# Kernel tuning notes

Hardware: AMD Instinct MI355X
Metric: run time of the kernel (lower is better)

The kernel has to match this reference:

```python
import jax, jax.numpy as jnp
import numpy as np
import math

B, T_TOK, D, H, L, V, NC, BS = 8, 511, 768, 12, 8, 512, 10, 512

PARAM_NAMES = ['tok_emb','cond_emb','type_emb','pos_emb','ln1_g','ln1_b','Wq','bq','Wk','bk','Wv','bv','Wp','bp','ln2_g','ln2_b','W1','b1','W2','b2','lnf_g','lnf_b','head_w']


def setup_inputs() -> dict:
    key = jax.random.key(0)
    ks = iter(jax.random.split(key, 40))
    def w(shape):
        return jax.random.normal(next(ks), shape, jnp.float32) * 0.02
    inp = {
        'idx': jax.random.randint(next(ks), (B, T_TOK), 0, V),
        'condition': jax.random.randint(next(ks), (B,), 0, NC + 1),
        'tok_emb': w((V, D)),
        'cond_emb': w((NC + 1, D)),
        'type_emb': w((2, D)),
        'pos_emb': w((1, BS, D)),
        'ln1_g': jnp.ones((L, D)), 'ln1_b': jnp.zeros((L, D)),
        'Wq': w((L, D, D)), 'bq': jnp.zeros((L, D)),
        'Wk': w((L, D, D)), 'bk': jnp.zeros((L, D)),
        'Wv': w((L, D, D)), 'bv': jnp.zeros((L, D)),
        'Wp': w((L, D, D)), 'bp': jnp.zeros((L, D)),
        'ln2_g': jnp.ones((L, D)), 'ln2_b': jnp.zeros((L, D)),
        'W1': w((L, D, 4 * D)), 'b1': jnp.zeros((L, 4 * D)),
        'W2': w((L, 4 * D, D)), 'b2': jnp.zeros((L, D)),
        'lnf_g': jnp.ones((D,)), 'lnf_b': jnp.zeros((D,)),
        'head_w': w((D, V)),
    }
    return inp


def _ln(x, g, b):
    m = x.mean(-1, keepdims=True)
    v = ((x - m) ** 2).mean(-1, keepdims=True)
    return (x - m) * jax.lax.rsqrt(v + 1e-5) * g + b


def _forward(idx, condition, p):
    b, t = idx.shape
    T = t + 1  # conditioning token prepended
    x = jnp.concatenate([p['cond_emb'][condition][:, None, :], p['tok_emb'][idx]], axis=1)
    type_ids = jnp.concatenate([jnp.zeros((1,), jnp.int32), jnp.ones((t,), jnp.int32)])
    x = x + p['pos_emb'][:, :T] + p['type_emb'][type_ids][None]
    dh = D // H
    causal = jnp.tril(jnp.ones((T, T), bool))

    def block(x, lp):
        ln1_g, ln1_b, Wq, bq, Wk, bk, Wv, bv, Wp, bp, ln2_g, ln2_b, W1, b1, W2, b2 = lp
        h = _ln(x, ln1_g, ln1_b)
        def heads(W, bias):
            return (h @ W + bias).reshape(b, T, H, dh).transpose(0, 2, 1, 3)  # [b,H,T,dh]
        q, k, v = heads(Wq, bq), heads(Wk, bk), heads(Wv, bv)
        att = jnp.einsum('bhqd,bhkd->bhqk', q, k) * (1.0 / math.sqrt(dh))
        att = jax.nn.softmax(jnp.where(causal, att, -jnp.inf), axis=-1)
        y = jnp.einsum('bhqk,bhkd->bhqd', att, v).transpose(0, 2, 1, 3).reshape(b, T, D)
        # NOTE: original Block applies ln1 in-place, so residual base is post-ln h
        x = h + (y @ Wp + bp)
        h2 = _ln(x, ln2_g, ln2_b)
        x = x + (jax.nn.gelu(h2 @ W1 + b1, approximate=False) @ W2 + b2)
        return x, None

    lp = (p['ln1_g'], p['ln1_b'], p['Wq'], p['bq'], p['Wk'], p['bk'], p['Wv'], p['bv'],
          p['Wp'], p['bp'], p['ln2_g'], p['ln2_b'], p['W1'], p['b1'], p['W2'], p['b2'])
    x, _ = jax.lax.scan(block, x, lp)
    logits = _ln(x, p['lnf_g'], p['lnf_b']) @ p['head_w']
    return logits[:, 1:, :]  # strip conditioning position (cond_len=1)


def reference(idx, condition, tok_emb, cond_emb, type_emb, pos_emb, ln1_g, ln1_b, Wq, bq, Wk, bk, Wv, bv, Wp, bp, ln2_g, ln2_b, W1, b1, W2, b2, lnf_g, lnf_b, head_w):
    p = dict(zip(PARAM_NAMES, (tok_emb, cond_emb, type_emb, pos_emb, ln1_g, ln1_b, Wq, bq, Wk, bk, Wv, bv, Wp, bp, ln2_g, ln2_b, W1, b1, W2, b2, lnf_g, lnf_b, head_w)))
    return _forward(idx, condition, p)
```

## Files before the change

kernel.cpp:

```cpp
#include <hip/hip_runtime.h>
#include <hip/hip_bf16.h>
#include <cstddef>
#include <cstdint>


#define NTOK 4096
#define TSEQ 512
#define DMODEL 768
#define DFF 3072
#define NHEAD 12
#define DHEAD 64
#define NLAYER 8
#define VOCAB 512
#define QKVD 2304

typedef __attribute__((ext_vector_type(8))) __bf16 bf16x8;
typedef __attribute__((ext_vector_type(4))) float f32x4;
typedef __attribute__((ext_vector_type(4))) unsigned int u32x4;
typedef __attribute__((ext_vector_type(4))) unsigned short u16x4;

__device__ __forceinline__ unsigned short f2bf(float f) {
  union { float f; unsigned int u; } v; v.f = f;
  return (unsigned short)((v.u + 0x7FFFu + ((v.u >> 16) & 1u)) >> 16);
}

__device__ __forceinline__ float gelu_exact(float x) {
  return 0.5f * x * (1.f + erff(x * 0.70710678118654752f));
}

__device__ __forceinline__ void gload_lds16(const void* g, void* lds) {
  __builtin_amdgcn_global_load_lds(
      reinterpret_cast<__attribute__((address_space(1))) void*>(
          reinterpret_cast<uintptr_t>(g)),
      reinterpret_cast<__attribute__((address_space(3))) void*>(
          reinterpret_cast<uintptr_t>(lds)),
      16, 0, 0);
}

template <int N>
__device__ __forceinline__ void waitvm() {
  if constexpr (N == 0) asm volatile("s_waitcnt vmcnt(0)" ::: "memory");
  else if constexpr (N == 2) asm volatile("s_waitcnt vmcnt(2)" ::: "memory");
  else if constexpr (N == 3) asm volatile("s_waitcnt vmcnt(3)" ::: "memory");
  else if constexpr (N == 4) asm volatile("s_waitcnt vmcnt(4)" ::: "memory");
  else static_assert(N == 0, "unsupported vmcnt");
}

__global__ __launch_bounds__(256) void embed_k(
    const int* __restrict__ idx, const int* __restrict__ cond,
    const float* __restrict__ tok, const float* __restrict__ ce,
    const float* __restrict__ te, const float* __restrict__ pe,
    float* __restrict__ X) {
  int row = blockIdx.x;
  int b = row >> 9, t = row & 511;
  int tid = threadIdx.x;
  const float* src = (t == 0) ? (ce + (size_t)cond[b] * DMODEL)
                              : (tok + (size_t)idx[b * 511 + t - 1] * DMODEL);
  const float* ty = te + (t != 0 ? DMODEL : 0);
  const float* pp = pe + (size_t)t * DMODEL;
  float* dst = X + (size_t)row * DMODEL;
#pragma unroll
  for (int i = 0; i < 3; i++) {
    int d = tid + i * 256;
    dst[d] = src[d] + pp[d] + ty[d];
  }
}

template <bool F32OUT>
__global__ __launch_bounds__(256) void ln_k(
    const float* __restrict__ X, const float* __restrict__ g,
    const float* __restrict__ bta, float* __restrict__ O,
    unsigned short* __restrict__ Ob) {
  const int row = blockIdx.x;
  const int tid = threadIdx.x;
  const float* x = X + (size_t)row * DMODEL;
  float v0 = x[tid], v1 = x[tid + 256], v2 = x[tid + 512];
  float s = v0 + v1 + v2;
  float ss = v0 * v0 + v1 * v1 + v2 * v2;
#pragma unroll
  for (int o = 32; o > 0; o >>= 1) {
    s += __shfl_down(s, o);
    ss += __shfl_down(ss, o);
  }
  __shared__ float sm[8];
  const int wid = tid >> 6, lane = tid & 63;
  if (lane == 0) { sm[wid] = s; sm[wid + 4] = ss; }
  __syncthreads();
  float st = sm[0] + sm[1] + sm[2] + sm[3];
  float sst = sm[4] + sm[5] + sm[6] + sm[7];
  float mean = st * (1.f / DMODEL);
  float var = sst * (1.f / DMODEL) - mean * mean;
  float rstd = rsqrtf(var + 1e-5f);
  float y0 = (v0 - mean) * rstd * g[tid] + bta[tid];
  float y1 = (v1 - mean) * rstd * g[tid + 256] + bta[tid + 256];
  float y2 = (v2 - mean) * rstd * g[tid + 512] + bta[tid + 512];
  if (F32OUT) {
    float* o = O + (size_t)row * DMODEL;
    o[tid] = y0; o[tid + 256] = y1; o[tid + 512] = y2;
  }
  unsigned short* ob = Ob + (size_t)row * DMODEL;
  ob[tid] = f2bf(y0); ob[tid + 256] = f2bf(y1); ob[tid + 512] = f2bf(y2);
}

struct P4 { const float* p[4]; };

__global__ __launch_bounds__(256) void transp_k(P4 src,
                                                unsigned short* __restrict__ out,
                                                int K, int N) {
  __shared__ alignas(16) float Ls[64][65];
  const float* W = src.p[blockIdx.z];
  unsigned short* o = out + (size_t)blockIdx.z * K * N;
  const int tid = threadIdx.x;
  const int n0 = blockIdx.x * 64, k0 = blockIdx.y * 64;
  const int r = tid >> 4, c4 = (tid & 15) * 4;
#pragma unroll
  for (int i = 0; i < 4; i++) {
    const int kk = r + i * 16;
    const float4 v = *(const float4*)(W + (size_t)(k0 + kk) * N + n0 + c4);
    Ls[c4 + 0][kk] = v.x;
    Ls[c4 + 1][kk] = v.y;
    Ls[c4 + 2][kk] = v.z;
    Ls[c4 + 3][kk] = v.w;
  }
  __syncthreads();
#pragma unroll
  for (int i = 0; i < 4; i++) {
    const int nn = r + i * 16;
    u16x4 q;
    q.x = f2bf(Ls[nn][c4 + 0]);
    q.y = f2bf(Ls[nn][c4 + 1]);
    q.z = f2bf(Ls[nn][c4 + 2]);
    q.w = f2bf(Ls[nn][c4 + 3]);
    *(u16x4*)(o + (size_t)(n0 + nn) * K + k0 + c4) = q;
  }
}

__global__ __launch_bounds__(256) void packb_k(const float* __restrict__ bq,
                                               const float* __restrict__ bk,
                                               const float* __restrict__ bv,
                                               float* __restrict__ o) {
  const int l = blockIdx.x, tid = threadIdx.x;
#pragma unroll
  for (int i = 0; i < 9; i++) {
    int n = tid + i * 256;
    float v = (n < 768) ? bq[l * 768 + n]
                        : (n < 1536) ? bk[l * 768 + n - 768]
                                     : bv[l * 768 + n - 1536];
    o[l * QKVD + n] = v;
  }
}

#define BK 32

constexpr int EPQ = 0;
constexpr int EPRES = 1;
constexpr int EPGELU = 2;
constexpr int EPHEAD = 3;
constexpr int EPQB = 4;

template <int EP, int TBM, int TBN>
__global__ __launch_bounds__(256) void mm_k(
    const unsigned short* __restrict__ A, const unsigned short* __restrict__ Bt,
    const float* __restrict__ bias, const float* __restrict__ res,
    void* __restrict__ Cv, int K, int N) {
  __shared__ alignas(16) unsigned short As[3][TBM * BK];
  __shared__ alignas(16) unsigned short Bs[3][TBN * BK];
  constexpr int WM = TBM / 2, WN = TBN / 2;
  constexpr int MI = WM / 16, NJ = WN / 16;
  constexpr int GA = TBM / 64, GB = TBN / 64;
  constexpr int G = GA + GB;
  const int tid = threadIdx.x;
  const int lane = tid & 63, wid = tid >> 6;
  const int wr = wid >> 1, wc = wid & 1;
  const int m0 = blockIdx.x * TBM, n0 = blockIdx.y * TBN;

  f32x4 acc[MI][NJ];
#pragma unroll
  for (int i = 0; i < MI; i++)
#pragma unroll
    for (int j = 0; j < NJ; j++) acc[i][j] = f32x4{0.f, 0.f, 0.f, 0.f};

  const int srow = lane >> 2;
  const int gch = (lane & 3) ^ ((srow >> 1) & 3);
  const size_t rb = (size_t)K * 2;
  const int fr = lane & 15, ks = lane >> 4;
  const int NKI = K / BK;

  auto stage = [&](int kt, int slot) {
    const size_t koff = (size_t)kt * BK * 2;
#pragma unroll
    for (int t = 0; t < GA; t++) {
      const int rr = wid * (TBM / 4) + t * 16;
      gload_lds16((const char*)A + (size_t)(m0 + rr + srow) * rb + koff + gch * 16,
                  &As[slot][rr * BK]);
    }
#pragma unroll
    for (int t = 0; t < GB; t++) {
      const int rr = wid * (TBN / 4) + t * 16;
      gload_lds16((const char*)Bt + (size_t)(n0 + rr + srow) * rb + koff + gch * 16,
                  &Bs[slot][rr * BK]);
    }
  };

  stage(0, 0);
  stage(1, 1);
  waitvm<G>();
  __builtin_amdgcn_s_barrier();
  __builtin_amdgcn_sched_barrier(0);

  int cur = 0;
  for (int t = 0; t < NKI; ++t) {
    const unsigned short* Ab = &As[cur][0];
    const unsigned short* Bb = &Bs[cur][0];
    u32x4 ar[MI], br[NJ];
#pragma unroll
    for (int i = 0; i < MI; i++) {
      const int ra = wr * WM + i * 16 + fr;
      ar[i] = *(const u32x4*)((const char*)Ab + ra * 64 +
                              ((ks ^ ((ra >> 1) & 3)) << 4));
    }
#pragma unroll
    for (int j = 0; j < NJ; j++) {
      const int rbw = wc * WN + j * 16 + fr;
      br[j] = *(const u32x4*)((const char*)Bb + rbw * 64 +
                              ((ks ^ ((rbw >> 1) & 3)) << 4));
    }
    const int nslot = (cur >= 1) ? cur - 1 : cur + 2;
    const bool pf = (t + 2 < NKI);
    if (pf) stage(t + 2, nslot);
    __builtin_amdgcn_s_setprio(1);
#pragma unroll
    for (int i = 0; i < MI; i++)
#pragma unroll
      for (int j = 0; j < NJ; j++)
        acc[i][j] = __builtin_amdgcn_mfma_f32_16x16x32_bf16(
            __builtin_bit_cast(bf16x8, ar[i]), __builtin_bit_cast(bf16x8, br[j]),
            acc[i][j], 0, 0, 0);
    __builtin_amdgcn_s_setprio(0);
    if (pf) waitvm<G>(); else waitvm<0>();
    __builtin_amdgcn_sched_barrier(0);
    __builtin_amdgcn_s_barrier();
    __builtin_amdgcn_sched_barrier(0);
    cur = (cur == 2) ? 0 : cur + 1;
  }

#pragma unroll
  for (int i = 0; i < MI; i++) {
#pragma unroll
    for (int j = 0; j < NJ; j++) {
      const int n = n0 + wc * WN + j * 16 + fr;
      float bv = 0.f;
      if (EP != EPHEAD) bv = bias[n];
#pragma unroll
      for (int r = 0; r < 4; r++) {
        const int m = m0 + wr * WM + i * 16 + ks * 4 + r;
        float v = acc[i][j][r] + bv;
        if (EP == EPRES) v += res[(size_t)m * N + n];
        if (EP == EPGELU) {
          ((unsigned short*)Cv)[(size_t)m * N + n] = f2bf(gelu_exact(v));
        } else if (EP == EPQB) {
          ((unsigned short*)Cv)[(size_t)m * N + n] = f2bf(v);
        } else if (EP == EPHEAD) {
          const int bb = m >> 9, tt = m & 511;
          if (tt)
            ((float*)Cv)[(size_t)(bb * 511 + tt - 1) * N + n] = v;
        } else {
          ((float*)Cv)[(size_t)m * N + n] = v;
        }
      }
    }
  }
}

__global__ __launch_bounds__(256) void attn_mfma_k(
    const unsigned short* __restrict__ QKV, unsigned short* __restrict__ Y) {
  __shared__ alignas(16) unsigned short Ks[64][72];
  __shared__ alignas(16) unsigned short Vt[64][72];
  __shared__ alignas(16) unsigned short Pl[4][16][72];
  const int qt = 7 - (int)blockIdx.x;
  const int h = blockIdx.y, b = blockIdx.z;
  const int tid = threadIdx.x;
  const int lane = tid & 63, wq = tid >> 6;
  const int fr = lane & 15, g = lane >> 4;

  const size_t qrow =
      (size_t)(b * TSEQ + qt * 64 + wq * 16 + fr) * QKVD + h * DHEAD;
  u32x4 qf[2];
  qf[0] = *(const u32x4*)(QKV + qrow + g * 8);
  qf[1] = *(const u32x4*)(QKV + qrow + 32 + g * 8);

  f32x4 of[4];
  float m[4], l[4];
#pragma unroll
  for (int jd = 0; jd < 4; jd++) of[jd] = f32x4{0.f, 0.f, 0.f, 0.f};
#pragma unroll
  for (int r = 0; r < 4; r++) { m[r] = -1e30f; l[r] = 0.f; }

  const int srow = tid >> 2, sc = (tid & 3) * 16;

  for (int kt = 0; kt <= qt; kt++) {
    {
      const size_t kr = (size_t)(b * TSEQ + kt * 64 + srow) * QKVD + h * DHEAD;
      u32x4 k0 = *(const u32x4*)(QKV + kr + DMODEL + sc);
      u32x4 k1 = *(const u32x4*)(QKV + kr + DMODEL + sc + 8);
      *(u32x4*)&Ks[srow][sc] = k0;
      *(u32x4*)&Ks[srow][sc + 8] = k1;
      u32x4 v0 = *(const u32x4*)(QKV + kr + 2 * DMODEL + sc);
      u32x4 v1 = *(const u32x4*)(QKV + kr + 2 * DMODEL + sc + 8);
      const unsigned short* vp = (const unsigned short*)&v0;
#pragma unroll
      for (int i = 0; i < 8; i++) Vt[sc + i][srow] = vp[i];
      vp = (const unsigned short*)&v1;
#pragma unroll
      for (int i = 0; i < 8; i++) Vt[sc + 8 + i][srow] = vp[i];
    }
    __syncthreads();

    f32x4 sf[4];
#pragma unroll
    for (int j = 0; j < 4; j++) sf[j] = f32x4{0.f, 0.f, 0.f, 0.f};
#pragma unroll
    for (int st = 0; st < 2; st++) {
#pragma unroll
      for (int j = 0; j < 4; j++) {
        u32x4 kf = *(const u32x4*)&Ks[j * 16 + fr][st * 32 + g * 8];
        sf[j] = __builtin_amdgcn_mfma_f32_16x16x32_bf16(
            __builtin_bit_cast(bf16x8, qf[st]), __builtin_bit_cast(bf16x8, kf),
            sf[j], 0, 0, 0);
      }
    }

    const bool diag = (kt == qt);
#pragma unroll
    for (int r = 0; r < 4; r++) {
      float pv[4];
      float mx = -1e30f;
#pragma unroll
      for (int j = 0; j < 4; j++) {
        float sv = sf[j][r] * 0.125f;
        if (diag && (j * 16 + fr > wq * 16 + g * 4 + r)) sv = -1e30f;
        pv[j] = sv;
        mx = fmaxf(mx, sv);
      }
      mx = fmaxf(mx, __shfl_xor(mx, 1));
      mx = fmaxf(mx, __shfl_xor(mx, 2));
      mx = fmaxf(mx, __shfl_xor(mx, 4));
      mx = fmaxf(mx, __shfl_xor(mx, 8));
      const float mn = fmaxf(m[r], mx);
      const float corr = __expf(m[r] - mn);
      m[r] = mn;
      float ls = 0.f;
#pragma unroll
      for (int j = 0; j < 4; j++) {
        const float e = __expf(pv[j] - mn);
        Pl[wq][g * 4 + r][j * 16 + fr] = f2bf(e);
        ls += e;
      }
      ls += __shfl_xor(ls, 1);
      ls += __shfl_xor(ls, 2);
      ls += __shfl_xor(ls, 4);
      ls += __shfl_xor(ls, 8);
      l[r] = l[r] * corr + ls;
#pragma unroll
      for (int jd = 0; jd < 4; jd++) of[jd][r] *= corr;
    }

#pragma unroll
    for (int st = 0; st < 2; st++) {
      u32x4 pf = *(const u32x4*)&Pl[wq][fr][st * 32 + g * 8];
#pragma unroll
      for (int jd = 0; jd < 4; jd++) {
        u32x4 vf = *(const u32x4*)&Vt[jd * 16 + fr][st * 32 + g * 8];
        of[jd] = __builtin_amdgcn_mfma_f32_16x16x32_bf16(
            __builtin_bit_cast(bf16x8, pf), __builtin_bit_cast(bf16x8, vf),
            of[jd], 0, 0, 0);
      }
    }
    __syncthreads();
  }

#pragma unroll
  for (int r = 0; r < 4; r++) {
    const float inv = 1.f / l[r];
    const size_t orow =
        (size_t)(b * TSEQ + qt * 64 + wq * 16 + g * 4 + r) * DMODEL + h * DHEAD;
#pragma unroll
    for (int jd = 0; jd < 4; jd++)
      Y[orow + jd * 16 + fr] = f2bf(of[jd][r] * inv);
  }
}

extern "C" void kernel_launch(void* const* d_in, const int* in_sizes, int n_in,
                              void* d_out, int out_size, void* d_ws, size_t ws_size,
                              hipStream_t stream) {
  const int* idx = (const int*)d_in[0];
  const int* condition = (const int*)d_in[1];
  const float* tok_emb = (const float*)d_in[2];
  const float* cond_emb = (const float*)d_in[3];
  const float* type_emb = (const float*)d_in[4];
  const float* pos_emb = (const float*)d_in[5];
  const float* ln1_g = (const float*)d_in[6];
  const float* ln1_b = (const float*)d_in[7];
  const float* Wq = (const float*)d_in[8];
  const float* bq = (const float*)d_in[9];
  const float* Wk = (const float*)d_in[10];
  const float* bk = (const float*)d_in[11];
  const float* Wv = (const float*)d_in[12];
  const float* bv = (const float*)d_in[13];
  const float* Wp = (const float*)d_in[14];
  const float* bp = (const float*)d_in[15];
  const float* ln2_g = (const float*)d_in[16];
  const float* ln2_b = (const float*)d_in[17];
  const float* W1 = (const float*)d_in[18];
  const float* b1 = (const float*)d_in[19];
  const float* W2 = (const float*)d_in[20];
  const float* b2 = (const float*)d_in[21];
  const float* lnf_g = (const float*)d_in[22];
  const float* lnf_b = (const float*)d_in[23];
  const float* head_w = (const float*)d_in[24];

  const size_t WDD = (size_t)DMODEL * DMODEL;
  const size_t WDF = (size_t)DMODEL * DFF;
  const size_t SD = (size_t)NTOK * DMODEL;

  char* wp = (char*)d_ws;
  auto alloc = [&](size_t bytes) {
    char* r = wp;
    wp += (bytes + 255) & ~(size_t)255;
    return r;
  };
  float* x = (float*)alloc(SD * 4);
  float* h = (float*)alloc(SD * 4);
  unsigned short* hb = (unsigned short*)alloc(SD * 2);
  unsigned short* big = (unsigned short*)alloc((size_t)NTOK * DFF * 2);
  unsigned short* qkv16 = big;
  unsigned short* m1b = big;
  unsigned short* yb = (unsigned short*)alloc(SD * 2);
  unsigned short* lw = (unsigned short*)alloc((4 * WDD + 2 * WDF) * 2);
  unsigned short* headt = (unsigned short*)alloc((size_t)VOCAB * DMODEL * 2);
  float* qkvb = (float*)alloc((size_t)NLAYER * QKVD * 4);

  unsigned short* lwQKV = lw;
  unsigned short* lwP = lw + 3 * WDD;
  unsigned short* lw1 = lw + 4 * WDD;
  unsigned short* lw2 = lw + 4 * WDD + WDF;

  embed_k<<<NTOK, 256, 0, stream>>>(idx, condition, tok_emb, cond_emb,
                                    type_emb, pos_emb, x);
  packb_k<<<NLAYER, 256, 0, stream>>>(bq, bk, bv, qkvb);
  {
    P4 s{{head_w, nullptr, nullptr, nullptr}};
    transp_k<<<dim3(VOCAB / 64, DMODEL / 64, 1), 256, 0, stream>>>(
        s, headt, DMODEL, VOCAB);
  }

  const dim3 gQKV(NTOK / 128, QKVD / 128);
  const dim3 gDD(NTOK / 128, DMODEL / 64);
  const dim3 gDF(NTOK / 128, DFF / 128);
  const dim3 gDV(NTOK / 128, VOCAB / 64);

  for (int l = 0; l < NLAYER; l++) {
    {
      P4 s{{Wq + l * WDD, Wk + l * WDD, Wv + l * WDD, Wp + l * WDD}};
      transp_k<<<dim3(12, 12, 4), 256, 0, stream>>>(s, lw, DMODEL, DMODEL);
      P4 s1{{W1 + l * WDF, nullptr, nullptr, nullptr}};
      transp_k<<<dim3(48, 12, 1), 256, 0, stream>>>(s1, lw1, DMODEL, DFF);
      P4 s2{{W2 + l * WDF, nullptr, nullptr, nullptr}};
      transp_k<<<dim3(12, 48, 1), 256, 0, stream>>>(s2, lw2, DFF, DMODEL);
    }
    ln_k<true><<<NTOK, 256, 0, stream>>>(x, ln1_g + l * DMODEL,
                                         ln1_b + l * DMODEL, h, hb);
    mm_k<EPQB, 128, 128><<<gQKV, 256, 0, stream>>>(
        hb, lwQKV, qkvb + l * QKVD, nullptr, qkv16, DMODEL, QKVD);
    attn_mfma_k<<<dim3(8, NHEAD, 8), 256, 0, stream>>>(qkv16, yb);
    mm_k<EPRES, 128, 64><<<gDD, 256, 0, stream>>>(
        yb, lwP, bp + l * DMODEL, h, x, DMODEL, DMODEL);
    ln_k<false><<<NTOK, 256, 0, stream>>>(x, ln2_g + l * DMODEL,
                                          ln2_b + l * DMODEL, nullptr, hb);
    mm_k<EPGELU, 128, 128><<<gDF, 256, 0, stream>>>(
        hb, lw1, b1 + l * DFF, nullptr, m1b, DMODEL, DFF);
    mm_k<EPRES, 128, 64><<<gDD, 256, 0, stream>>>(
        m1b, lw2, b2 + l * DMODEL, x, x, DFF, DMODEL);
  }

  ln_k<false><<<NTOK, 256, 0, stream>>>(x, lnf_g, lnf_b, nullptr, hb);
  mm_k<EPHEAD, 128, 64><<<gDV, 256, 0, stream>>>(
      hb, headt, nullptr, nullptr, d_out, DMODEL, VOCAB);
}
```

Measured before the change: 1.559 ms.

## Batch weight transposes across layers and add single-buffer GEMM variant

Weight transposes for all layers are launched up front in three large kernels when the workspace is big enough, replacing 24 small per-layer launches. The GEMM kernel gains a PIPE template parameter: the 128x128 QKV and FFN1 GEMMs now use a single-buffered load/sync loop with less LDS, which may raise occupancy. The 128x64 GEMMs keep the triple-buffered pipeline. The trade-off is a larger workspace and the loss of load/compute overlap in the single-buffered GEMMs.

```diff
diff --git a/kernel.cpp b/kernel.cpp
--- a/kernel.cpp
+++ b/kernel.cpp
@@ -106,10 +106,13 @@
 
 __global__ __launch_bounds__(256) void transp_k(P4 src,
                                                 unsigned short* __restrict__ out,
-                                                int K, int N) {
+                                                int K, int N, long srcL,
+                                                long dstL, int matsPer) {
   __shared__ alignas(16) float Ls[64][65];
-  const float* W = src.p[blockIdx.z];
-  unsigned short* o = out + (size_t)blockIdx.z * K * N;
+  const int z = blockIdx.z;
+  const int l = z / matsPer, mt = z - l * matsPer;
+  const float* W = src.p[mt] + (size_t)l * srcL;
+  unsigned short* o = out + (size_t)l * dstL + (size_t)mt * K * N;
   const int tid = threadIdx.x;
   const int n0 = blockIdx.x * 64, k0 = blockIdx.y * 64;
   const int r = tid >> 4, c4 = (tid & 15) * 4;
@@ -158,13 +161,14 @@
 constexpr int EPHEAD = 3;
 constexpr int EPQB = 4;
 
-template <int EP, int TBM, int TBN>
+template <int EP, int TBM, int TBN, int PIPE>
 __global__ __launch_bounds__(256) void mm_k(
     const unsigned short* __restrict__ A, const unsigned short* __restrict__ Bt,
     const float* __restrict__ bias, const float* __restrict__ res,
     void* __restrict__ Cv, int K, int N) {
-  __shared__ alignas(16) unsigned short As[3][TBM * BK];
-  __shared__ alignas(16) unsigned short Bs[3][TBN * BK];
+  constexpr int NBUF = PIPE ? 3 : 1;
+  __shared__ alignas(16) unsigned short As[NBUF][TBM * BK];
+  __shared__ alignas(16) unsigned short Bs[NBUF][TBN * BK];
   constexpr int WM = TBM / 2, WN = TBN / 2;
   constexpr int MI = WM / 16, NJ = WN / 16;
   constexpr int GA = TBM / 64, GB = TBN / 64;
@@ -191,44 +195,33 @@
 #pragma unroll
     for (int t = 0; t < GA; t++) {
       const int rr = wid * (TBM / 4) + t * 16;
-      gload_lds16((const char*)A + (size_t)(m0 + rr + srow) * rb + koff + gch * 16,
+      gload_lds16((const char*)A + (size_t)(m0 + rr + srow) * rb + koff +
+                      gch * 16,
                   &As[slot][rr * BK]);
     }
 #pragma unroll
     for (int t = 0; t < GB; t++) {
       const int rr = wid * (TBN / 4) + t * 16;
-      gload_lds16((const char*)Bt + (size_t)(n0 + rr + srow) * rb + koff + gch * 16,
+      gload_lds16((const char*)Bt + (size_t)(n0 + rr + srow) * rb + koff +
+                      gch * 16,
                   &Bs[slot][rr * BK]);
     }
   };
 
-  stage(0, 0);
-  stage(1, 1);
-  waitvm<G>();
-  __builtin_amdgcn_s_barrier();
-  __builtin_amdgcn_sched_barrier(0);
-
-  int cur = 0;
-  for (int t = 0; t < NKI; ++t) {
-    const unsigned short* Ab = &As[cur][0];
-    const unsigned short* Bb = &Bs[cur][0];
+  auto frags_mfma = [&](int slot) {
     u32x4 ar[MI], br[NJ];
 #pragma unroll
     for (int i = 0; i < MI; i++) {
       const int ra = wr * WM + i * 16 + fr;
-      ar[i] = *(const u32x4*)((const char*)Ab + ra * 64 +
+      ar[i] = *(const u32x4*)((const char*)&As[slot][0] + ra * 64 +
                               ((ks ^ ((ra >> 1) & 3)) << 4));
     }
 #pragma unroll
     for (int j = 0; j < NJ; j++) {
       const int rbw = wc * WN + j * 16 + fr;
-      br[j] = *(const u32x4*)((const char*)Bb + rbw * 64 +
+      br[j] = *(const u32x4*)((const char*)&Bs[slot][0] + rbw * 64 +
                               ((ks ^ ((rbw >> 1) & 3)) << 4));
     }
-    const int nslot = (cur >= 1) ? cur - 1 : cur + 2;
-    const bool pf = (t + 2 < NKI);
-    if (pf) stage(t + 2, nslot);
-    __builtin_amdgcn_s_setprio(1);
 #pragma unroll
     for (int i = 0; i < MI; i++)
 #pragma unroll
@@ -236,12 +229,54 @@
         acc[i][j] = __builtin_amdgcn_mfma_f32_16x16x32_bf16(
             __builtin_bit_cast(bf16x8, ar[i]), __builtin_bit_cast(bf16x8, br[j]),
             acc[i][j], 0, 0, 0);
-    __builtin_amdgcn_s_setprio(0);
-    if (pf) waitvm<G>(); else waitvm<0>();
-    __builtin_amdgcn_sched_barrier(0);
+  };
+
+  if (PIPE == 0) {
+    for (int t = 0; t < NKI; ++t) {
+      stage(t, 0);
+      __syncthreads();
+      frags_mfma(0);
+      __syncthreads();
+    }
+  } else {
+    stage(0, 0);
+    stage(1, 1);
+    waitvm<G>();
     __builtin_amdgcn_s_barrier();
     __builtin_amdgcn_sched_barrier(0);
-    cur = (cur == 2) ? 0 : cur + 1;
+    int cur = 0;
+    for (int t = 0; t < NKI; ++t) {
+      const int nslot = (cur >= 1) ? cur - 1 : cur + 2;
+      const bool pf = (t + 2 < NKI);
+      u32x4 ar[MI], br[NJ];
+#pragma unroll
+      for (int i = 0; i < MI; i++) {
+        const int ra = wr * WM + i * 16 + fr;
+        ar[i] = *(const u32x4*)((const char*)&As[cur][0] + ra * 64 +
+                                ((ks ^ ((ra >> 1) & 3)) << 4));
+      }
+#pragma unroll
+      for (int j = 0; j < NJ; j++) {
+        const int rbw = wc * WN + j * 16 + fr;
+        br[j] = *(const u32x4*)((const char*)&Bs[cur][0] + rbw * 64 +
+                                ((ks ^ ((rbw >> 1) & 3)) << 4));
+      }
+      if (pf) stage(t + 2, nslot);
+      __builtin_amdgcn_s_setprio(1);
+#pragma unroll
+      for (int i = 0; i < MI; i++)
+#pragma unroll
+        for (int j = 0; j < NJ; j++)
+          acc[i][j] = __builtin_amdgcn_mfma_f32_16x16x32_bf16(
+              __builtin_bit_cast(bf16x8, ar[i]),
+              __builtin_bit_cast(bf16x8, br[j]), acc[i][j], 0, 0, 0);
+      __builtin_amdgcn_s_setprio(0);
+      if (pf) waitvm<G>(); else waitvm<0>();
+      __builtin_amdgcn_sched_barrier(0);
+      __builtin_amdgcn_s_barrier();
+      __builtin_amdgcn_sched_barrier(0);
+      cur = (cur == 2) ? 0 : cur + 1;
+    }
   }
 
 #pragma unroll
@@ -422,6 +457,7 @@
   const size_t WDD = (size_t)DMODEL * DMODEL;
   const size_t WDF = (size_t)DMODEL * DFF;
   const size_t SD = (size_t)NTOK * DMODEL;
+  const size_t LW = 4 * WDD + 2 * WDF;
 
   char* wp = (char*)d_ws;
   auto alloc = [&](size_t bytes) {
@@ -436,14 +472,11 @@
   unsigned short* qkv16 = big;
   unsigned short* m1b = big;
   unsigned short* yb = (unsigned short*)alloc(SD * 2);
-  unsigned short* lw = (unsigned short*)alloc((4 * WDD + 2 * WDF) * 2);
   unsigned short* headt = (unsigned short*)alloc((size_t)VOCAB * DMODEL * 2);
   float* qkvb = (float*)alloc((size_t)NLAYER * QKVD * 4);
-
-  unsigned short* lwQKV = lw;
-  unsigned short* lwP = lw + 3 * WDD;
-  unsigned short* lw1 = lw + 4 * WDD;
-  unsigned short* lw2 = lw + 4 * WDD + WDF;
+  const size_t fixedB = (size_t)(wp - (char*)d_ws);
+  const bool bigws = ws_size >= fixedB + NLAYER * LW * 2 + 65536;
+  unsigned short* lw = (unsigned short*)alloc((bigws ? NLAYER * LW : LW) * 2);
 
   embed_k<<<NTOK, 256, 0, stream>>>(idx, condition, tok_emb, cond_emb,
                                     type_emb, pos_emb, x);
@@ -451,7 +484,18 @@
   {
     P4 s{{head_w, nullptr, nullptr, nullptr}};
     transp_k<<<dim3(VOCAB / 64, DMODEL / 64, 1), 256, 0, stream>>>(
-        s, headt, DMODEL, VOCAB);
+        s, headt, DMODEL, VOCAB, 0, 0, 1);
+  }
+  if (bigws) {
+    P4 s{{Wq, Wk, Wv, Wp}};
+    transp_k<<<dim3(12, 12, 4 * NLAYER), 256, 0, stream>>>(
+        s, lw, DMODEL, DMODEL, (long)WDD, (long)LW, 4);
+    P4 s1{{W1, nullptr, nullptr, nullptr}};
+    transp_k<<<dim3(48, 12, NLAYER), 256, 0, stream>>>(
+        s1, lw + 4 * WDD, DMODEL, DFF, (long)WDF, (long)LW, 1);
+    P4 s2{{W2, nullptr, nullptr, nullptr}};
+    transp_k<<<dim3(12, 48, NLAYER), 256, 0, stream>>>(
+        s2, lw + 4 * WDD + WDF, DFF, DMODEL, (long)WDF, (long)LW, 1);
   }
 
   const dim3 gQKV(NTOK / 128, QKVD / 128);
@@ -460,30 +504,38 @@
   const dim3 gDV(NTOK / 128, VOCAB / 64);
 
   for (int l = 0; l < NLAYER; l++) {
-    {
+    unsigned short* lwL = lw + (bigws ? l * LW : 0);
+    unsigned short* lwQKV = lwL;
+    unsigned short* lwP = lwL + 3 * WDD;
+    unsigned short* lw1 = lwL + 4 * WDD;
+    unsigned short* lw2 = lwL + 4 * WDD + WDF;
+    if (!bigws) {
       P4 s{{Wq + l * WDD, Wk + l * WDD, Wv + l * WDD, Wp + l * WDD}};
-      transp_k<<<dim3(12, 12, 4), 256, 0, stream>>>(s, lw, DMODEL, DMODEL);
+      transp_k<<<dim3(12, 12, 4), 256, 0, stream>>>(s, lwL, DMODEL, DMODEL, 0,
+                                                    0, 4);
       P4 s1{{W1 + l * WDF, nullptr, nullptr, nullptr}};
-      transp_k<<<dim3(48, 12, 1), 256, 0, stream>>>(s1, lw1, DMODEL, DFF);
+      transp_k<<<dim3(48, 12, 1), 256, 0, stream>>>(s1, lw1, DMODEL, DFF, 0, 0,
+                                                    1);
       P4 s2{{W2 + l * WDF, nullptr, nullptr, nullptr}};
-      transp_k<<<dim3(12, 48, 1), 256, 0, stream>>>(s2, lw2, DFF, DMODEL);
+      transp_k<<<dim3(12, 48, 1), 256, 0, stream>>>(s2, lw2, DFF, DMODEL, 0, 0,
+                                                    1);
     }
     ln_k<true><<<NTOK, 256, 0, stream>>>(x, ln1_g + l * DMODEL,
                                          ln1_b + l * DMODEL, h, hb);
-    mm_k<EPQB, 128, 128><<<gQKV, 256, 0, stream>>>(
+    mm_k<EPQB, 128, 128, 0><<<gQKV, 256, 0, stream>>>(
         hb, lwQKV, qkvb + l * QKVD, nullptr, qkv16, DMODEL, QKVD);
     attn_mfma_k<<<dim3(8, NHEAD, 8), 256, 0, stream>>>(qkv16, yb);
-    mm_k<EPRES, 128, 64><<<gDD, 256, 0, stream>>>(
+    mm_k<EPRES, 128, 64, 1><<<gDD, 256, 0, stream>>>(
         yb, lwP, bp + l * DMODEL, h, x, DMODEL, DMODEL);
     ln_k<false><<<NTOK, 256, 0, stream>>>(x, ln2_g + l * DMODEL,
                                           ln2_b + l * DMODEL, nullptr, hb);
-    mm_k<EPGELU, 128, 128><<<gDF, 256, 0, stream>>>(
+    mm_k<EPGELU, 128, 128, 0><<<gDF, 256, 0, stream>>>(
         hb, lw1, b1 + l * DFF, nullptr, m1b, DMODEL, DFF);
-    mm_k<EPRES, 128, 64><<<gDD, 256, 0, stream>>>(
+    mm_k<EPRES, 128, 64, 1><<<gDD, 256, 0, stream>>>(
         m1b, lw2, b2 + l * DMODEL, x, x, DFF, DMODEL);
   }
 
   ln_k<false><<<NTOK, 256, 0, stream>>>(x, lnf_g, lnf_b, nullptr, hb);
-  mm_k<EPHEAD, 128, 64><<<gDV, 256, 0, stream>>>(
+  mm_k<EPHEAD, 128, 64, 1><<<gDV, 256, 0, stream>>>(
       hb, headt, nullptr, nullptr, d_out, DMODEL, VOCAB);
 }
```

Measured after the change: 1.598 ms. +2.5%, slower.
